# Performance work log

Hardware: AMD Instinct MI355X
Metric: run time of the kernel (lower is better)

## Reference

```python
import jax, jax.numpy as jnp
import numpy as np


def setup_inputs() -> dict:
    key = jax.random.key(0)
    k1, k2 = jax.random.split(key)
    B, L, N = 32, 256, 1024
    x = jax.random.normal(k1, (B, L, N), dtype=jnp.float32)
    # glorot-uniform [L, L]
    limit = float(np.sqrt(6.0 / (L + L)))
    weight = jax.random.uniform(k2, (L, L), dtype=jnp.float32, minval=-limit, maxval=limit)
    bias = jnp.zeros((L,), dtype=jnp.float32)
    return {"x": x, "weight": weight, "bias": bias}


def _ada_gcn(xn, weight, bias):
    # xn: [N, B, L] node-major features
    N, B, L = xn.shape
    # L2-normalize features, mean cosine similarity over batch -> [N, N]
    x_norm = xn / jnp.maximum(jnp.linalg.norm(xn, axis=-1, keepdims=True), 1e-12)
    mean_sim = jnp.einsum('nbl,mbl->nm', x_norm, x_norm) / B
    k = max(int(N * 0.3), 1)
    _, idx = jax.lax.top_k(mean_sim, k + 1)          # [N, k+1]
    rows = jnp.arange(N)[:, None]
    non_self = idx != rows
    order = jnp.cumsum(non_self.astype(jnp.int32), axis=1) - 1
    keep = non_self & (order < k)                     # first k non-self neighbors
    mask = jnp.zeros((N, N), dtype=bool).at[jnp.broadcast_to(rows, idx.shape), idx].set(keep)
    # A[src, dst]: dst kept as neighbor of src, weighted by mean similarity
    A = jnp.where(mask, mean_sim, jnp.zeros((), mean_sim.dtype))
    # gcn_norm (no self loops): deg over dst, symmetric normalization
    deg = A.sum(axis=0)                               # [N] in-degree by weight
    dinv = jnp.where(deg > 0, jax.lax.rsqrt(deg), jnp.zeros((), deg.dtype))
    An = dinv[:, None] * A * dinv[None, :]
    # feature transform + weighted scatter-add aggregation out[dst] += w * x[src]
    xw = jnp.einsum('nbl,lo->nbo', xn, weight)
    out = jnp.einsum('sd,sbl->dbl', An, xw) + bias
    return out


def reference(x, weight, bias):
    # x: [B, L, N] -> node-major [N, B, L]
    xn = jnp.transpose(x, (2, 0, 1))
    num_levels = 1
    for _ in range(num_levels):
        xn = _ada_gcn(xn, weight, bias)
    return jnp.transpose(xn, (1, 2, 0))  # [B, L, N]
```

## Files before the change

### kernel.cpp

```cpp
#include <hip/hip_runtime.h>

#define BB 32
#define LL 256
#define NN 1024
#define BL 8192
#define TOPK 307
#define SPLITK 16
#define NTILES 36
#define PART_STRIDE ((size_t)NTILES * 16384)

typedef unsigned short ushort_t;
typedef unsigned long long u64;
typedef __bf16 bf16x8 __attribute__((ext_vector_type(8)));
typedef float f32x4 __attribute__((ext_vector_type(4)));
typedef unsigned short us4 __attribute__((ext_vector_type(4)));

__device__ __forceinline__ ushort_t f2bf(float f) {
    unsigned int u = __float_as_uint(f);
    u += 0x7FFFu + ((u >> 16) & 1u);
    return (ushort_t)(u >> 16);
}
__device__ __forceinline__ float bf2f(ushort_t h) {
    return __uint_as_float(((unsigned int)h) << 16);
}

__device__ __forceinline__ void gload16(const void* g, const void* l) {
    __builtin_amdgcn_global_load_lds(
        (__attribute__((address_space(1))) void*)(unsigned long long)g,
        (__attribute__((address_space(3))) void*)(unsigned int)(unsigned long long)l,
        16, 0, 0);
}


__global__ __launch_bounds__(256) void k_prep(const float* __restrict__ x,
                                              ushort_t* __restrict__ xhi,
                                              ushort_t* __restrict__ xlo,
                                              float* __restrict__ nrm,
                                              const float* __restrict__ W,
                                              ushort_t* __restrict__ WT) {
    __shared__ float tile[32][268];
    __shared__ float red[32][33];
    __shared__ float inv[32];
    __shared__ float wt[32][33];
    const int t = threadIdx.x;
    if (blockIdx.x == 32) {
        const int tx = t & 31, ty = t >> 5;
#pragma unroll
        for (int s = 0; s < 2; ++s) {
            const int id = blockIdx.y * 2 + s;
            const int c0 = (id & 7) * 32;
            const int r0 = (id >> 3) * 32;
#pragma unroll
            for (int j = 0; j < 32; j += 8)
                wt[ty + j][tx] = W[(size_t)(r0 + ty + j) * LL + c0 + tx];
            __syncthreads();
#pragma unroll
            for (int j = 0; j < 32; j += 8)
                WT[(size_t)(c0 + ty + j) * LL + r0 + tx] = f2bf(wt[tx][ty + j]);
            __syncthreads();
        }
        return;
    }
    const int n0 = blockIdx.x * 32, b = blockIdx.y;
    const int qn = (t & 7) * 4, lr = t >> 3;
    const float* xb = x + (size_t)b * LL * NN + n0;
    float p0 = 0.f, p1 = 0.f, p2 = 0.f, p3 = 0.f;
#pragma unroll
    for (int j = 0; j < 8; ++j) {
        int l = lr + 32 * j;
        f32x4 v = *(const f32x4*)&xb[(size_t)l * NN + qn];
        tile[qn + 0][l] = v[0];
        tile[qn + 1][l] = v[1];
        tile[qn + 2][l] = v[2];
        tile[qn + 3][l] = v[3];
        p0 = fmaf(v[0], v[0], p0);
        p1 = fmaf(v[1], v[1], p1);
        p2 = fmaf(v[2], v[2], p2);
        p3 = fmaf(v[3], v[3], p3);
    }
    red[lr][qn + 0] = p0;
    red[lr][qn + 1] = p1;
    red[lr][qn + 2] = p2;
    red[lr][qn + 3] = p3;
    __syncthreads();
    if (t < 32) {
        float acc = 0.f;
#pragma unroll
        for (int j = 0; j < 32; ++j) acc += red[j][t];
        float nv = fmaxf(sqrtf(acc), 1e-12f);
        nrm[b * NN + n0 + t] = nv;
        inv[t] = 1.0f / nv;
    }
    __syncthreads();
    const int l4 = (t & 63) * 4, wv = t >> 6;
#pragma unroll
    for (int j = 0; j < 8; ++j) {
        const int nl = wv * 8 + j;
        f32x4 v = *(const f32x4*)&tile[nl][l4];
        const float iv = inv[nl];
        us4 hi, lo;
#pragma unroll
        for (int i = 0; i < 4; ++i) {
            float sc = v[i] * iv;
            ushort_t h = f2bf(sc);
            hi[i] = h;
            lo[i] = f2bf(sc - bf2f(h));
        }
        size_t o = (size_t)(n0 + nl) * BL + b * LL + l4;
        *(us4*)&xhi[o] = hi;
        *(us4*)&xlo[o] = lo;
    }
}

__global__ __launch_bounds__(256, 2) void k_sim_mfma(const ushort_t* __restrict__ Xhi,
                                                     const ushort_t* __restrict__ Xlo,
                                                     float* __restrict__ part) {
    __shared__ ushort_t sAh[2][4096], sAl[2][4096];
    __shared__ ushort_t sBh[2][4096], sBl[2][4096];
    const int t = threadIdx.x, l = t & 63, w = t >> 6;
    const int bid = blockIdx.x;
    const int swz = (bid & 7) * 72 + (bid >> 3);
    const int z = swz / NTILES;
    const int tid36 = swz - z * NTILES;
    int id = tid36, ti = 0;
    while (id >= 8 - ti) { id -= 8 - ti; ++ti; }
    const int tj = ti + id;
    const int i0 = ti * 128, j0 = tj * 128;
    const int it0 = 16 * z, it1 = it0 + 16;
    const int ra = t >> 2;
    const int rb = ra + 64;
    const int qa = ((((t & 3) - (ra >> 1)) & 3)) * 8;
    const int lb0 = 512 * w, lb1 = 512 * (w + 4);
    const int wr = (w >> 1) * 64, wc = (w & 1) * 64;
    const int lrow = l & 15, g = l >> 4;
    const ushort_t* Ah = Xhi + (size_t)i0 * BL;
    const ushort_t* Al = Xlo + (size_t)i0 * BL;
    const ushort_t* Bh = Xhi + (size_t)j0 * BL;
    const ushort_t* Bl = Xlo + (size_t)j0 * BL;

    int offA[4], offB[4];
#pragma unroll
    for (int r = 0; r < 4; ++r) {
        int row = wr + r * 16 + lrow;
        offA[r] = row * 32 + (((g + (row >> 1)) & 3) * 8);
        row = wc + r * 16 + lrow;
        offB[r] = row * 32 + (((g + (row >> 1)) & 3) * 8);
    }

    auto dma = [&](int it, int buf) {
        const int k0 = it * 32;
        gload16(Ah + (size_t)ra * BL + k0 + qa, &sAh[buf][lb0]);
        gload16(Ah + (size_t)rb * BL + k0 + qa, &sAh[buf][lb1]);
        gload16(Al + (size_t)ra * BL + k0 + qa, &sAl[buf][lb0]);
        gload16(Al + (size_t)rb * BL + k0 + qa, &sAl[buf][lb1]);
        gload16(Bh + (size_t)ra * BL + k0 + qa, &sBh[buf][lb0]);
        gload16(Bh + (size_t)rb * BL + k0 + qa, &sBh[buf][lb1]);
        gload16(Bl + (size_t)ra * BL + k0 + qa, &sBl[buf][lb0]);
        gload16(Bl + (size_t)rb * BL + k0 + qa, &sBl[buf][lb1]);
    };

    f32x4 acc[4][4] = {};
    dma(it0, 0);
    for (int it = it0; it < it1; ++it) {
        const int cur = (it - it0) & 1;
        __syncthreads();
        if (it + 1 < it1) dma(it + 1, cur ^ 1);
        bf16x8 ah[4], al[4], bh[4], bl[4];
#pragma unroll
        for (int r = 0; r < 4; ++r) {
            ah[r] = *(const bf16x8*)&sAh[cur][offA[r]];
            al[r] = *(const bf16x8*)&sAl[cur][offA[r]];
        }
#pragma unroll
        for (int c = 0; c < 4; ++c) {
            bh[c] = *(const bf16x8*)&sBh[cur][offB[c]];
            bl[c] = *(const bf16x8*)&sBl[cur][offB[c]];
        }
#pragma unroll
        for (int r = 0; r < 4; ++r)
#pragma unroll
            for (int c = 0; c < 4; ++c) {
                acc[r][c] = __builtin_amdgcn_mfma_f32_16x16x32_bf16(ah[r], bh[c], acc[r][c], 0, 0, 0);
                acc[r][c] = __builtin_amdgcn_mfma_f32_16x16x32_bf16(ah[r], bl[c], acc[r][c], 0, 0, 0);
                acc[r][c] = __builtin_amdgcn_mfma_f32_16x16x32_bf16(al[r], bh[c], acc[r][c], 0, 0, 0);
            }
    }
    float* P = part + (size_t)z * PART_STRIDE + (size_t)tid36 * 16384;
    const int orow = wr + (l >> 4) * 4;
    const int ocol = wc + lrow;
#pragma unroll
    for (int r = 0; r < 4; ++r)
#pragma unroll
        for (int c = 0; c < 4; ++c)
#pragma unroll
            for (int p = 0; p < 4; ++p)
                P[(size_t)(orow + r * 16 + p) * 128 + ocol + c * 16] = acc[r][c][p];
}

__global__ __launch_bounds__(256) void k_reduce(const float* __restrict__ part,
                                                float* __restrict__ sim) {
    __shared__ float tl[64][65];
    const int t = threadIdx.x;
    int id = blockIdx.x, ti = 0;
    while (id >= 8 - ti) { id -= 8 - ti; ++ti; }
    const int tj = ti + id;
    const int q = blockIdx.y;
    const int r0 = (q >> 1) * 64, c0 = (q & 1) * 64;
    const float* Pu = part + (size_t)blockIdx.x * 16384;
    const int fr = t & 15, rq = t >> 4;
#pragma unroll
    for (int e = 0; e < 4; ++e) {
        int r = e * 16 + rq;
        f32x4 s = {};
#pragma unroll
        for (int z = 0; z < SPLITK; ++z)
            s += *(const f32x4*)&Pu[(size_t)z * PART_STRIDE + (size_t)(r0 + r) * 128 + c0 + fr * 4];
        s *= (1.0f / BB);
        *(f32x4*)&sim[(size_t)(ti * 128 + r0 + r) * NN + tj * 128 + c0 + fr * 4] = s;
        tl[r][fr * 4 + 0] = s[0];
        tl[r][fr * 4 + 1] = s[1];
        tl[r][fr * 4 + 2] = s[2];
        tl[r][fr * 4 + 3] = s[3];
    }
    __syncthreads();
    if (ti != tj) {
#pragma unroll
        for (int e = 0; e < 16; ++e) {
            int li = e * 256 + t;
            int cc = li >> 6, rr = li & 63;
            sim[(size_t)(tj * 128 + c0 + cc) * NN + ti * 128 + r0 + rr] = tl[rr][cc];
        }
    }
}

#define FOR16(M) M(0) M(1) M(2) M(3) M(4) M(5) M(6) M(7) \
                 M(8) M(9) M(10) M(11) M(12) M(13) M(14) M(15)
__global__ __launch_bounds__(256, 1) void k_topk(const float* __restrict__ sim,
                                                 float* __restrict__ A,
                                                 float* __restrict__ deg) {
    const int t = threadIdx.x, l = t & 63, w = t >> 6;
    if (blockIdx.x == 0) {
        f32x4 zz = {};
        *(f32x4*)&deg[t * 4] = zz;
    }
    const int n = blockIdx.x * 4 + w;
    const float* row = sim + (size_t)n * NN + l * 16;
    f32x4 v0 = *(const f32x4*)(row + 0);
    f32x4 v1 = *(const f32x4*)(row + 4);
    f32x4 v2 = *(const f32x4*)(row + 8);
    f32x4 v3 = *(const f32x4*)(row + 12);
    const int selfe = n - l * 16;
#define MKK(i, vec, c) unsigned k##i; { unsigned u = __float_as_uint(vec[c]); \
    unsigned kk = (u & 0x80000000u) ? ~u : (u | 0x80000000u); \
    k##i = (selfe == i) ? 0u : kk; }
    MKK(0, v0, 0)  MKK(1, v0, 1)  MKK(2, v0, 2)  MKK(3, v0, 3)
    MKK(4, v1, 0)  MKK(5, v1, 1)  MKK(6, v1, 2)  MKK(7, v1, 3)
    MKK(8, v2, 0)  MKK(9, v2, 1)  MKK(10, v2, 2) MKK(11, v2, 3)
    MKK(12, v3, 0) MKK(13, v3, 1) MKK(14, v3, 2) MKK(15, v3, 3)
#undef MKK
    unsigned cur = 0u;
    for (int bit = 31; bit >= 0; --bit) {
        unsigned cand = cur | (1u << bit);
        int c = 0;
#define CNT(i) c += __popcll(__ballot(k##i >= cand));
        FOR16(CNT)
#undef CNT
        if (c >= TOPK) cur = cand;
    }
    const unsigned T = cur;
    int cgt = 0;
#define CGT(i) cgt += __popcll(__ballot(k##i > T));
    FOR16(CGT)
#undef CGT
    const int need = TOPK - cgt;
    const u64 mymask = (l == 0) ? 0ull : (~0ull >> (64 - l));
    int base = 0;
    f32x4 o0, o1, o2, o3;
#define EMT(i, vec, c, ov, oc) { u64 beq = __ballot(k##i == T); \
    int rank = base + __popcll(beq & mymask); \
    bool keep = (k##i > T) | ((k##i == T) & (rank < need)); \
    ov[oc] = keep ? vec[c] : 0.0f; \
    base += __popcll(beq); }
    EMT(0, v0, 0, o0, 0)  EMT(1, v0, 1, o0, 1)  EMT(2, v0, 2, o0, 2)  EMT(3, v0, 3, o0, 3)
    EMT(4, v1, 0, o1, 0)  EMT(5, v1, 1, o1, 1)  EMT(6, v1, 2, o1, 2)  EMT(7, v1, 3, o1, 3)
    EMT(8, v2, 0, o2, 0)  EMT(9, v2, 1, o2, 1)  EMT(10, v2, 2, o2, 2) EMT(11, v2, 3, o2, 3)
    EMT(12, v3, 0, o3, 0) EMT(13, v3, 1, o3, 1) EMT(14, v3, 2, o3, 2) EMT(15, v3, 3, o3, 3)
#undef EMT
    float* Ar = A + (size_t)n * NN + l * 16;
    *(f32x4*)(Ar + 0)  = o0;
    *(f32x4*)(Ar + 4)  = o1;
    *(f32x4*)(Ar + 8)  = o2;
    *(f32x4*)(Ar + 12) = o3;
}

__global__ __launch_bounds__(256) void k_deg(const float* __restrict__ A,
                                             float* __restrict__ deg) {
    const int t = threadIdx.x;
    const int r0 = blockIdx.x * 32;
    f32x4 a = {};
#pragma unroll 4
    for (int r = 0; r < 32; ++r)
        a += *(const f32x4*)&A[(size_t)(r0 + r) * NN + t * 4];
    atomicAdd(&deg[t * 4 + 0], a[0]);
    atomicAdd(&deg[t * 4 + 1], a[1]);
    atomicAdd(&deg[t * 4 + 2], a[2]);
    atomicAdd(&deg[t * 4 + 3], a[3]);
}

__global__ __launch_bounds__(256) void k_prescale_tr(const float* __restrict__ A,
                                                     const float* __restrict__ deg,
                                                     ushort_t* __restrict__ Atr) {
    __shared__ float tile[32][33];
    int c0 = blockIdx.x * 32;
    int r0 = blockIdx.y * 32;
    int tx = threadIdx.x, ty = threadIdx.y;
#pragma unroll
    for (int j = 0; j < 32; j += 8)
        tile[ty + j][tx] = A[(size_t)(r0 + ty + j) * NN + c0 + tx];
    __syncthreads();
#pragma unroll
    for (int j = 0; j < 32; j += 8) {
        int d = c0 + ty + j;
        int s = r0 + tx;
        float dd = deg[d], ds_ = deg[s];
        float di = (dd > 0.f) ? (1.0f / sqrtf(dd)) : 0.0f;
        float si = (ds_ > 0.f) ? (1.0f / sqrtf(ds_)) : 0.0f;
        Atr[(size_t)d * NN + s] = f2bf(tile[tx][ty + j] * di * si);
    }
}

__global__ __launch_bounds__(256, 4) void k_mfma_nt(const ushort_t* __restrict__ A,
                                                    const ushort_t* __restrict__ B,
                                                    void* __restrict__ Cv,
                                                    const float* __restrict__ bias,
                                                    const float* __restrict__ cscale,
                                                    int lda, int ldb, int ldc,
                                                    long strA, long strB, long strC,
                                                    int K, int bf16out) {
    __shared__ ushort_t sA[2][4096], sB[2][4096];
    const int t = threadIdx.x, l = t & 63, w = t >> 6;
    const int i0 = blockIdx.y * 128, j0 = blockIdx.x * 128, z = blockIdx.z;
    const ushort_t* Ab = A + (size_t)z * strA;
    const ushort_t* Bb = B + (size_t)z * strB;
    const int ra = t >> 2;
    const int rb = ra + 64;
    const int qa = ((((t & 3) - (ra >> 1)) & 3)) * 8;
    const int lb0 = 512 * w, lb1 = 512 * (w + 4);
    const int wr = (w >> 1) * 64, wc = (w & 1) * 64;
    const int lrow = l & 15, g = l >> 4;

    int offA[4], offB[4];
#pragma unroll
    for (int r = 0; r < 4; ++r) {
        int row = wr + r * 16 + lrow;
        offA[r] = row * 32 + (((g + (row >> 1)) & 3) * 8);
        row = wc + r * 16 + lrow;
        offB[r] = row * 32 + (((g + (row >> 1)) & 3) * 8);
    }

    auto dma = [&](int k0, int buf) {
        gload16(Ab + (size_t)(i0 + ra) * lda + k0 + qa, &sA[buf][lb0]);
        gload16(Ab + (size_t)(i0 + rb) * lda + k0 + qa, &sA[buf][lb1]);
        gload16(Bb + (size_t)(j0 + ra) * ldb + k0 + qa, &sB[buf][lb0]);
        gload16(Bb + (size_t)(j0 + rb) * ldb + k0 + qa, &sB[buf][lb1]);
    };

    f32x4 acc[4][4] = {};
    dma(0, 0);
    for (int k0 = 0; k0 < K; k0 += 32) {
        const int cur = (k0 >> 5) & 1;
        __syncthreads();
        if (k0 + 32 < K) dma(k0 + 32, cur ^ 1);
        bf16x8 af[4], bf_[4];
#pragma unroll
        for (int r = 0; r < 4; ++r)
            af[r] = *(const bf16x8*)&sA[cur][offA[r]];
#pragma unroll
        for (int c = 0; c < 4; ++c)
            bf_[c] = *(const bf16x8*)&sB[cur][offB[c]];
#pragma unroll
        for (int r = 0; r < 4; ++r)
#pragma unroll
            for (int c = 0; c < 4; ++c)
                acc[r][c] = __builtin_amdgcn_mfma_f32_16x16x32_bf16(af[r], bf_[c], acc[r][c], 0, 0, 0);
    }
    const int orow = i0 + wr + (l >> 4) * 4;
    const int ocol = j0 + wc + lrow;
    if (bf16out) {
        ushort_t* Cp = (ushort_t*)Cv + (size_t)z * strC;
#pragma unroll
        for (int c = 0; c < 4; ++c) {
            float sc = cscale ? cscale[(size_t)z * NN + ocol + c * 16] : 1.0f;
#pragma unroll
            for (int r = 0; r < 4; ++r)
#pragma unroll
                for (int p = 0; p < 4; ++p)
                    Cp[(size_t)(orow + r * 16 + p) * ldc + ocol + c * 16] = f2bf(acc[r][c][p] * sc);
        }
    } else {
        float* Cp = (float*)Cv + (size_t)z * strC;
#pragma unroll
        for (int r = 0; r < 4; ++r)
#pragma unroll
            for (int c = 0; c < 4; ++c)
#pragma unroll
                for (int p = 0; p < 4; ++p) {
                    float bv = bias ? bias[(orow + r * 16 + p) & (LL - 1)] : 0.0f;
                    Cp[(size_t)(orow + r * 16 + p) * ldc + ocol + c * 16] = acc[r][c][p] + bv;
                }
    }
}

extern "C" void kernel_launch(void* const* d_in, const int* in_sizes, int n_in,
                              void* d_out, int out_size, void* d_ws, size_t ws_size,
                              hipStream_t stream) {
    const float* x      = (const float*)d_in[0];
    const float* weight = (const float*)d_in[1];
    const float* bias   = (const float*)d_in[2];
    float* out = (float*)d_out;

    char* p = (char*)d_ws;
    ushort_t* xhi  = (ushort_t*)p; p += (size_t)NN * BL * 2;
    ushort_t* xlo  = (ushort_t*)p; p += (size_t)NN * BL * 2;
    float*    part = (float*)p;
    ushort_t* xwT  = (ushort_t*)p;
    p += (size_t)SPLITK * PART_STRIDE * 4;
    ushort_t* Atrb = (ushort_t*)p; p += (size_t)NN * NN * 2;
    ushort_t* WTb  = (ushort_t*)p; p += (size_t)LL * LL * 2;
    float* sim  = (float*)p; p += (size_t)NN * NN * 4;
    float* Aw   = (float*)p; p += (size_t)NN * NN * 4;
    float* deg  = (float*)p; p += NN * 4;
    float* nrm  = (float*)p; p += (size_t)BB * NN * 4;

    k_prep<<<dim3(NN / 32 + 1, BB), dim3(256), 0, stream>>>(x, xhi, xlo, nrm, weight, WTb);
    k_sim_mfma<<<dim3(NTILES * SPLITK), 256, 0, stream>>>(xhi, xlo, part);
    k_reduce<<<dim3(NTILES, 4), 256, 0, stream>>>(part, sim);
    k_topk<<<dim3(NN / 4), 256, 0, stream>>>(sim, Aw, deg);
    k_deg<<<dim3(NN / 32), 256, 0, stream>>>(Aw, deg);
    k_prescale_tr<<<dim3(NN / 32, NN / 32), dim3(32, 8), 0, stream>>>(Aw, deg, Atrb);
    k_mfma_nt<<<dim3(NN / 128, LL / 128, BB), 256, 0, stream>>>(
        WTb, xhi, xwT, nullptr, nrm, LL, BL, NN, 0, LL, (long)LL * NN, LL, 1);
    k_mfma_nt<<<dim3(NN / 128, BL / 128, 1), 256, 0, stream>>>(
        xwT, Atrb, out, bias, nullptr, NN, NN, NN, 0, 0, 0, NN, 0);
}
```

Before: 190.6 us.

## Split bf16x3 sim GEMM into three sequential passes to halve LDS and registers

The split-bf16 similarity GEMM now runs three separate K-loops (hi*hi, hi*lo, lo*hi), each streaming one A and one B operand. Before, it loaded hi and lo for both operands in a single loop. This halves the shared-memory buffers and fragment registers, and launch bounds go from 2 to 5 blocks per CU to raise occupancy. The cost is that global loads grow from 4 tile streams to 6 and the loop and sync overhead is tripled.

```diff
diff --git a/kernel.cpp b/kernel.cpp
--- a/kernel.cpp
+++ b/kernel.cpp
@@ -112,11 +112,10 @@
     }
 }
 
-__global__ __launch_bounds__(256, 2) void k_sim_mfma(const ushort_t* __restrict__ Xhi,
+__global__ __launch_bounds__(256, 5) void k_sim_mfma(const ushort_t* __restrict__ Xhi,
                                                      const ushort_t* __restrict__ Xlo,
                                                      float* __restrict__ part) {
-    __shared__ ushort_t sAh[2][4096], sAl[2][4096];
-    __shared__ ushort_t sBh[2][4096], sBl[2][4096];
+    __shared__ ushort_t sA[2][4096], sB[2][4096];
     const int t = threadIdx.x, l = t & 63, w = t >> 6;
     const int bid = blockIdx.x;
     const int swz = (bid & 7) * 72 + (bid >> 3);
@@ -147,43 +146,38 @@
         offB[r] = row * 32 + (((g + (row >> 1)) & 3) * 8);
     }
 
-    auto dma = [&](int it, int buf) {
+    auto dma = [&](const ushort_t* pa, const ushort_t* pb, int it, int buf) {
         const int k0 = it * 32;
-        gload16(Ah + (size_t)ra * BL + k0 + qa, &sAh[buf][lb0]);
-        gload16(Ah + (size_t)rb * BL + k0 + qa, &sAh[buf][lb1]);
-        gload16(Al + (size_t)ra * BL + k0 + qa, &sAl[buf][lb0]);
-        gload16(Al + (size_t)rb * BL + k0 + qa, &sAl[buf][lb1]);
-        gload16(Bh + (size_t)ra * BL + k0 + qa, &sBh[buf][lb0]);
-        gload16(Bh + (size_t)rb * BL + k0 + qa, &sBh[buf][lb1]);
-        gload16(Bl + (size_t)ra * BL + k0 + qa, &sBl[buf][lb0]);
-        gload16(Bl + (size_t)rb * BL + k0 + qa, &sBl[buf][lb1]);
+        gload16(pa + (size_t)ra * BL + k0 + qa, &sA[buf][lb0]);
+        gload16(pa + (size_t)rb * BL + k0 + qa, &sA[buf][lb1]);
+        gload16(pb + (size_t)ra * BL + k0 + qa, &sB[buf][lb0]);
+        gload16(pb + (size_t)rb * BL + k0 + qa, &sB[buf][lb1]);
     };
 
     f32x4 acc[4][4] = {};
-    dma(it0, 0);
-    for (int it = it0; it < it1; ++it) {
-        const int cur = (it - it0) & 1;
+#pragma unroll
+    for (int ph = 0; ph < 3; ++ph) {
+        const ushort_t* pa = (ph == 2) ? Al : Ah;
+        const ushort_t* pb = (ph == 1) ? Bl : Bh;
         __syncthreads();
-        if (it + 1 < it1) dma(it + 1, cur ^ 1);
-        bf16x8 ah[4], al[4], bh[4], bl[4];
-#pragma unroll
-        for (int r = 0; r < 4; ++r) {
-            ah[r] = *(const bf16x8*)&sAh[cur][offA[r]];
-            al[r] = *(const bf16x8*)&sAl[cur][offA[r]];
+        dma(pa, pb, it0, 0);
+        for (int it = it0; it < it1; ++it) {
+            const int cur = (it - it0) & 1;
+            __syncthreads();
+            if (it + 1 < it1) dma(pa, pb, it + 1, cur ^ 1);
+            bf16x8 af[4], bf_[4];
+#pragma unroll
+            for (int r = 0; r < 4; ++r)
+                af[r] = *(const bf16x8*)&sA[cur][offA[r]];
+#pragma unroll
+            for (int c = 0; c < 4; ++c)
+                bf_[c] = *(const bf16x8*)&sB[cur][offB[c]];
+#pragma unroll
+            for (int r = 0; r < 4; ++r)
+#pragma unroll
+                for (int c = 0; c < 4; ++c)
+                    acc[r][c] = __builtin_amdgcn_mfma_f32_16x16x32_bf16(af[r], bf_[c], acc[r][c], 0, 0, 0);
         }
-#pragma unroll
-        for (int c = 0; c < 4; ++c) {
-            bh[c] = *(const bf16x8*)&sBh[cur][offB[c]];
-            bl[c] = *(const bf16x8*)&sBl[cur][offB[c]];
-        }
-#pragma unroll
-        for (int r = 0; r < 4; ++r)
-#pragma unroll
-            for (int c = 0; c < 4; ++c) {
-                acc[r][c] = __builtin_amdgcn_mfma_f32_16x16x32_bf16(ah[r], bh[c], acc[r][c], 0, 0, 0);
-                acc[r][c] = __builtin_amdgcn_mfma_f32_16x16x32_bf16(ah[r], bl[c], acc[r][c], 0, 0, 0);
-                acc[r][c] = __builtin_amdgcn_mfma_f32_16x16x32_bf16(al[r], bh[c], acc[r][c], 0, 0, 0);
-            }
     }
     float* P = part + (size_t)z * PART_STRIDE + (size_t)tid36 * 16384;
     const int orow = wr + (l >> 4) * 4;
```

New measurement: 259.4 us. 1.36x slower.
